# Optimization experiments

Hardware: AMD Instinct MI355X
Metric: run time of the kernel (lower is better)

Reference implementation:

```python
import jax, jax.numpy as jnp
import numpy as np

N_NODES = 50000
N_EDGES = 800000
IN, HID, OUT = 96, 96, 64


def setup_inputs() -> dict:
    key = jax.random.key(0)
    ks = jax.random.split(key, 12)
    x = jax.random.normal(ks[0], (N_NODES, IN), dtype=jnp.float32)
    src = jax.random.randint(ks[1], (N_EDGES,), 0, N_NODES, dtype=jnp.int32)
    dst = jax.random.randint(ks[2], (N_EDGES,), 0, N_NODES, dtype=jnp.int32)
    dims = [(IN, HID), (HID, HID), (HID, OUT)]
    params = {}
    for i, (din, dout) in enumerate(dims):
        s = 1.0 / np.sqrt(din)
        params[f"w_self{i}"] = jax.random.uniform(ks[3 + 3 * i], (dout, din), jnp.float32, -s, s)
        params[f"w_neigh{i}"] = jax.random.uniform(ks[4 + 3 * i], (dout, din), jnp.float32, -s, s)
        params[f"b{i}"] = jnp.zeros((dout,), jnp.float32)
    return {"x": x, "src": src, "dst": dst, **params}


def _sage_layer(h, src, dst, w_self, w_neigh, b):
    # mean aggregation of source-node features onto destination nodes
    msum = jax.ops.segment_sum(h[src], dst, num_segments=N_NODES)  # [N, d]
    deg = jax.ops.segment_sum(jnp.ones((src.shape[0],), h.dtype), dst, num_segments=N_NODES)
    hmean = msum / jnp.maximum(deg, 1.0)[:, None]
    return h @ w_self.T + hmean @ w_neigh.T + b


def reference(x, src, dst,
              w_self0, w_neigh0, b0,
              w_self1, w_neigh1, b1,
              w_self2, w_neigh2, b2):
    # Layer 0 + ReLU (dropout is identity in eval mode)
    h = jax.nn.relu(_sage_layer(x, src, dst, w_self0, w_neigh0, b0))
    # Layer 1 + ReLU
    h = jax.nn.relu(_sage_layer(h, src, dst, w_self1, w_neigh1, b1))
    # Final layer, no activation
    h = _sage_layer(h, src, dst, w_self2, w_neigh2, b2)
    return h
```

## Files before the change

### kernel.cpp

```cpp
#include <hip/hip_runtime.h>
#include <hip/hip_fp16.h>


#define DIN 96

typedef __attribute__((ext_vector_type(8))) short bf16x8;
typedef __attribute__((ext_vector_type(16))) float f32x16;

__global__ void zero_deg_kernel(int* __restrict__ p, int n) {
    int i = blockIdx.x * blockDim.x + threadIdx.x;
    if (i < n) p[i] = 0;
}

__global__ void deg_kernel(const int* __restrict__ dst, int* __restrict__ deg,
                           int* __restrict__ rank, int nE) {
    int i = blockIdx.x * blockDim.x + threadIdx.x;
    if (i < nE) rank[i] = atomicAdd(&deg[dst[i]], 1);
}

__global__ void block_sum_kernel(const int* __restrict__ deg, int* __restrict__ bsum, int nN) {
    __shared__ int s[256];
    const int tid = threadIdx.x;
    int i = blockIdx.x * 256 + tid;
    s[tid] = (i < nN) ? deg[i] : 0;
    __syncthreads();
    for (int d = 128; d > 0; d >>= 1) {
        if (tid < d) s[tid] += s[tid + d];
        __syncthreads();
    }
    if (tid == 0) bsum[blockIdx.x] = s[0];
}

__global__ void bsum_scan_kernel(int* __restrict__ bsum, int nB) {
    __shared__ int s[256];
    const int tid = threadIdx.x;
    int v = (tid < nB) ? bsum[tid] : 0;
    s[tid] = v;
    __syncthreads();
    for (int d = 1; d < 256; d <<= 1) {
        int t = (tid >= d) ? s[tid - d] : 0;
        __syncthreads();
        s[tid] += t;
        __syncthreads();
    }
    if (tid < nB) bsum[tid] = s[tid] - v;
}

__global__ void scan_apply_kernel(const int* __restrict__ deg, const int* __restrict__ bsum,
                                  int* __restrict__ offs, int nN) {
    __shared__ int s[256];
    const int tid = threadIdx.x;
    int i = blockIdx.x * 256 + tid;
    int v = (i < nN) ? deg[i] : 0;
    s[tid] = v;
    __syncthreads();
    for (int d = 1; d < 256; d <<= 1) {
        int t = (tid >= d) ? s[tid - d] : 0;
        __syncthreads();
        s[tid] += t;
        __syncthreads();
    }
    if (i < nN) offs[i] = bsum[blockIdx.x] + s[tid] - v;
}

__global__ void bucket_kernel(const int* __restrict__ src, const int* __restrict__ dst,
                              const int* __restrict__ offs, const int* __restrict__ rank,
                              unsigned short* __restrict__ esrc, int nE) {
    int e = blockIdx.x * blockDim.x + threadIdx.x;
    if (e < nE) esrc[offs[dst[e]] + rank[e]] = (unsigned short)src[e];
}

__global__ void tof16_kernel(const float* __restrict__ x, __half* __restrict__ xf, int n8) {
    int i = blockIdx.x * blockDim.x + threadIdx.x;
    if (i >= n8) return;
    float4 f0 = *reinterpret_cast<const float4*>(x + (size_t)i * 8);
    float4 f1 = *reinterpret_cast<const float4*>(x + (size_t)i * 8 + 4);
    union { __half2 h2[4]; float4 raw; } o;
    o.h2[0] = __float22half2_rn(make_float2(f0.x, f0.y));
    o.h2[1] = __float22half2_rn(make_float2(f0.z, f0.w));
    o.h2[2] = __float22half2_rn(make_float2(f1.x, f1.y));
    o.h2[3] = __float22half2_rn(make_float2(f1.z, f1.w));
    *reinterpret_cast<float4*>(xf + (size_t)i * 8) = o.raw;
}

__global__ void gather_kernel(const __half* __restrict__ hf, const unsigned short* __restrict__ esrc,
                              const int* __restrict__ offs, const int* __restrict__ deg,
                              float* __restrict__ hmean, int nN) {
    int idx = blockIdx.x * blockDim.x + threadIdx.x;
    if (idx >= nN * 12) return;
    int n = idx / 12;
    int q = idx - n * 12;
    const int beg = offs[n];
    const int dg = deg[n];
    const int end = beg + dg;
    const __half* hq = hf + q * 8;

    union H8 { float4 raw; __half2 h2[4]; };
    float a0[8], a1[8], a2[8], a3[8];
#pragma unroll
    for (int k = 0; k < 8; ++k) { a0[k] = 0.f; a1[k] = 0.f; a2[k] = 0.f; a3[k] = 0.f; }

    int j = beg;
    for (; j + 4 <= end; j += 4) {
        int s0 = esrc[j], s1 = esrc[j + 1], s2 = esrc[j + 2], s3 = esrc[j + 3];
        H8 v0, v1, v2, v3;
        v0.raw = *reinterpret_cast<const float4*>(hq + (size_t)s0 * DIN);
        v1.raw = *reinterpret_cast<const float4*>(hq + (size_t)s1 * DIN);
        v2.raw = *reinterpret_cast<const float4*>(hq + (size_t)s2 * DIN);
        v3.raw = *reinterpret_cast<const float4*>(hq + (size_t)s3 * DIN);
#pragma unroll
        for (int k = 0; k < 4; ++k) {
            float2 f0 = __half22float2(v0.h2[k]);
            float2 f1 = __half22float2(v1.h2[k]);
            float2 f2 = __half22float2(v2.h2[k]);
            float2 f3 = __half22float2(v3.h2[k]);
            a0[2 * k] += f0.x; a0[2 * k + 1] += f0.y;
            a1[2 * k] += f1.x; a1[2 * k + 1] += f1.y;
            a2[2 * k] += f2.x; a2[2 * k + 1] += f2.y;
            a3[2 * k] += f3.x; a3[2 * k + 1] += f3.y;
        }
    }
    for (; j < end; ++j) {
        int s0 = esrc[j];
        H8 v0;
        v0.raw = *reinterpret_cast<const float4*>(hq + (size_t)s0 * DIN);
#pragma unroll
        for (int k = 0; k < 4; ++k) {
            float2 f0 = __half22float2(v0.h2[k]);
            a0[2 * k] += f0.x; a0[2 * k + 1] += f0.y;
        }
    }
    const float r = 1.0f / (float)max(dg, 1);
    float4 o0, o1;
    o0.x = (a0[0] + a1[0] + a2[0] + a3[0]) * r;
    o0.y = (a0[1] + a1[1] + a2[1] + a3[1]) * r;
    o0.z = (a0[2] + a1[2] + a2[2] + a3[2]) * r;
    o0.w = (a0[3] + a1[3] + a2[3] + a3[3]) * r;
    o1.x = (a0[4] + a1[4] + a2[4] + a3[4]) * r;
    o1.y = (a0[5] + a1[5] + a2[5] + a3[5]) * r;
    o1.z = (a0[6] + a1[6] + a2[6] + a3[6]) * r;
    o1.w = (a0[7] + a1[7] + a2[7] + a3[7]) * r;
    float* op = hmean + (size_t)n * DIN + q * 8;
    *reinterpret_cast<float4*>(op) = o0;
    *reinterpret_cast<float4*>(op + 4) = o1;
}

__device__ __forceinline__ void f32x8_to_hilo(const float4 f0, const float4 f1,
                                              bf16x8& hi, bf16x8& lo) {
    union { unsigned int u[4]; bf16x8 v; } H, L;
    const float fv[8] = {f0.x, f0.y, f0.z, f0.w, f1.x, f1.y, f1.z, f1.w};
#pragma unroll
    for (int i = 0; i < 4; ++i) {
        unsigned u0 = __float_as_uint(fv[2 * i]);
        unsigned u1 = __float_as_uint(fv[2 * i + 1]);
        unsigned h0 = u0 & 0xFFFF0000u;
        unsigned h1 = u1 & 0xFFFF0000u;
        H.u[i] = h1 | (h0 >> 16);
        float l0 = fv[2 * i]     - __uint_as_float(h0);
        float l1 = fv[2 * i + 1] - __uint_as_float(h1);
        L.u[i] = (__float_as_uint(l1) & 0xFFFF0000u) | (__float_as_uint(l0) >> 16);
    }
    hi = H.v; lo = L.v;
}

template<int DOUT, bool RELU, bool WF16>
__global__ __launch_bounds__(256)
void sage_gemm_mfma(const float* __restrict__ hin, const float* __restrict__ hmean,
                    const float* __restrict__ wself, const float* __restrict__ wneigh,
                    const float* __restrict__ bias, float* __restrict__ hout,
                    __half* __restrict__ fout, int nN) {
    __shared__ unsigned int WhiS[32][100];
    __shared__ unsigned int WloS[32][100];

    const int tid = threadIdx.x;
    const int n0 = blockIdx.x * 256;
    const int ob = blockIdx.y * 32;

    for (int c = tid; c < 32 * 24; c += 256) {
        int r = c / 24, k8 = c - (c / 24) * 24;
        const float* srcw = (k8 < 12) ? (wself + (size_t)(ob + r) * 96 + k8 * 8)
                                      : (wneigh + (size_t)(ob + r) * 96 + (k8 - 12) * 8);
        float4 f0 = *reinterpret_cast<const float4*>(srcw);
        float4 f1 = *reinterpret_cast<const float4*>(srcw + 4);
        bf16x8 hi, lo;
        f32x8_to_hilo(f0, f1, hi, lo);
        *reinterpret_cast<bf16x8*>(&WhiS[r][k8 * 4]) = hi;
        *reinterpret_cast<bf16x8*>(&WloS[r][k8 * 4]) = lo;
    }
    __syncthreads();

    const int lane = tid & 63;
    const int w = tid >> 6;
    const int col = lane & 31;
    const int q = lane >> 5;
    const int mbase = n0 + w * 64;

    const int nA0 = min(mbase + col, nN - 1);
    const int nA1 = min(mbase + 32 + col, nN - 1);

    f32x16 acc0 = {};
    f32x16 acc1 = {};

#pragma unroll
    for (int ks = 0; ks < 12; ++ks) {
        const int kk = ks * 16 + q * 8;
        const float* s0;
        const float* s1;
        if (kk < 96) {
            s0 = hin + (size_t)nA0 * 96 + kk;
            s1 = hin + (size_t)nA1 * 96 + kk;
        } else {
            s0 = hmean + (size_t)nA0 * 96 + (kk - 96);
            s1 = hmean + (size_t)nA1 * 96 + (kk - 96);
        }
        float4 a00 = *reinterpret_cast<const float4*>(s0);
        float4 a01 = *reinterpret_cast<const float4*>(s0 + 4);
        float4 a10 = *reinterpret_cast<const float4*>(s1);
        float4 a11 = *reinterpret_cast<const float4*>(s1 + 4);
        bf16x8 ahi0, alo0, ahi1, alo1;
        f32x8_to_hilo(a00, a01, ahi0, alo0);
        f32x8_to_hilo(a10, a11, ahi1, alo1);

        const bf16x8 whi = *reinterpret_cast<const bf16x8*>(&WhiS[col][ks * 8 + q * 4]);
        const bf16x8 wlo = *reinterpret_cast<const bf16x8*>(&WloS[col][ks * 8 + q * 4]);

        acc0 = __builtin_amdgcn_mfma_f32_32x32x16_bf16(ahi0, whi, acc0, 0, 0, 0);
        acc0 = __builtin_amdgcn_mfma_f32_32x32x16_bf16(ahi0, wlo, acc0, 0, 0, 0);
        acc0 = __builtin_amdgcn_mfma_f32_32x32x16_bf16(alo0, whi, acc0, 0, 0, 0);
        acc1 = __builtin_amdgcn_mfma_f32_32x32x16_bf16(ahi1, whi, acc1, 0, 0, 0);
        acc1 = __builtin_amdgcn_mfma_f32_32x32x16_bf16(ahi1, wlo, acc1, 0, 0, 0);
        acc1 = __builtin_amdgcn_mfma_f32_32x32x16_bf16(alo1, whi, acc1, 0, 0, 0);
    }

    const float bv = bias[ob + col];
#pragma unroll
    for (int i = 0; i < 16; ++i) {
        const int row = (i & 3) + 8 * (i >> 2) + 4 * q;
        int n = mbase + row;
        if (n < nN) {
            float v = acc0[i] + bv;
            if (RELU) v = fmaxf(v, 0.f);
            hout[(size_t)n * DOUT + ob + col] = v;
            if (WF16) fout[(size_t)n * DOUT + ob + col] = __float2half_rn(v);
        }
        n = mbase + 32 + row;
        if (n < nN) {
            float v = acc1[i] + bv;
            if (RELU) v = fmaxf(v, 0.f);
            hout[(size_t)n * DOUT + ob + col] = v;
            if (WF16) fout[(size_t)n * DOUT + ob + col] = __float2half_rn(v);
        }
    }
}

extern "C" void kernel_launch(void* const* d_in, const int* in_sizes, int n_in,
                              void* d_out, int out_size, void* d_ws, size_t ws_size,
                              hipStream_t stream) {
    const float* x   = (const float*)d_in[0];
    const int*   src = (const int*)d_in[1];
    const int*   dst = (const int*)d_in[2];
    const float* ws0 = (const float*)d_in[3];
    const float* wn0 = (const float*)d_in[4];
    const float* b0  = (const float*)d_in[5];
    const float* ws1 = (const float*)d_in[6];
    const float* wn1 = (const float*)d_in[7];
    const float* b1  = (const float*)d_in[8];
    const float* ws2 = (const float*)d_in[9];
    const float* wn2 = (const float*)d_in[10];
    const float* b2  = (const float*)d_in[11];
    float* out = (float*)d_out;

    const int nN = in_sizes[0] / DIN;
    const int nE = in_sizes[1];
    const int nB = (nN + 255) / 256;

    int* deg  = (int*)d_ws;
    int* offs = deg + 50048;
    int* bsum = offs + 50048;
    int* rank = bsum + 256;
    unsigned short* esrc = (unsigned short*)(rank + nE);
    float* hmean = (float*)(esrc + nE);
    float* hA    = hmean + (size_t)nN * DIN;
    float* hB    = hA + (size_t)nN * DIN;

    __half* f16buf = (__half*)d_out;

    zero_deg_kernel<<<nB, 256, 0, stream>>>(deg, nN);
    deg_kernel<<<(nE + 255) / 256, 256, 0, stream>>>(dst, deg, rank, nE);
    block_sum_kernel<<<nB, 256, 0, stream>>>(deg, bsum, nN);
    bsum_scan_kernel<<<1, 256, 0, stream>>>(bsum, nB);
    scan_apply_kernel<<<nB, 256, 0, stream>>>(deg, bsum, offs, nN);
    bucket_kernel<<<(nE + 255) / 256, 256, 0, stream>>>(src, dst, offs, rank, esrc, nE);

    const int ggrid = (nN * 12 + 255) / 256;
    const int cgrid = (nN * 12 + 255) / 256;
    const int mblocks = (nN + 255) / 256;
    dim3 mgrid96(mblocks, 3);
    dim3 mgrid64(mblocks, 2);

    tof16_kernel<<<cgrid, 256, 0, stream>>>(x, f16buf, nN * 12);
    gather_kernel<<<ggrid, 256, 0, stream>>>(f16buf, esrc, offs, deg, hmean, nN);
    sage_gemm_mfma<96, true, true><<<mgrid96, 256, 0, stream>>>(x, hmean, ws0, wn0, b0, hA, f16buf, nN);

    gather_kernel<<<ggrid, 256, 0, stream>>>(f16buf, esrc, offs, deg, hmean, nN);
    sage_gemm_mfma<96, true, true><<<mgrid96, 256, 0, stream>>>(hA, hmean, ws1, wn1, b1, hB, f16buf, nN);

    gather_kernel<<<ggrid, 256, 0, stream>>>(f16buf, esrc, offs, deg, hmean, nN);
    sage_gemm_mfma<64, false, false><<<mgrid64, 256, 0, stream>>>(hB, hmean, ws2, wn2, b2, out, nullptr, nN);
}
```

Measured before the change: 228.2 us.

## Store neighbour mean in fp16 and compute all output columns per GEMM block

The gather kernel now writes the mean-aggregated features as fp16 instead of fp32, which halves its store traffic and the GEMM's hmean reads. The GEMM no longer splits output columns across blockIdx.y. Each block loads the full weight matrix into LDS and loops over all 32-column panels, so every A row is read and split into hi/lo parts once instead of 2-3 times. The cost is rounding the mean to fp16 before the bf16 hi/lo split, larger LDS use, more accumulator registers, and fewer blocks in flight.

```diff
diff --git a/kernel.cpp b/kernel.cpp
--- a/kernel.cpp
+++ b/kernel.cpp
@@ -85,7 +85,7 @@
 
 __global__ void gather_kernel(const __half* __restrict__ hf, const unsigned short* __restrict__ esrc,
                               const int* __restrict__ offs, const int* __restrict__ deg,
-                              float* __restrict__ hmean, int nN) {
+                              __half* __restrict__ hmean, int nN) {
     int idx = blockIdx.x * blockDim.x + threadIdx.x;
     if (idx >= nN * 12) return;
     int n = idx / 12;
@@ -131,24 +131,16 @@
         }
     }
     const float r = 1.0f / (float)max(dg, 1);
-    float4 o0, o1;
-    o0.x = (a0[0] + a1[0] + a2[0] + a3[0]) * r;
-    o0.y = (a0[1] + a1[1] + a2[1] + a3[1]) * r;
-    o0.z = (a0[2] + a1[2] + a2[2] + a3[2]) * r;
-    o0.w = (a0[3] + a1[3] + a2[3] + a3[3]) * r;
-    o1.x = (a0[4] + a1[4] + a2[4] + a3[4]) * r;
-    o1.y = (a0[5] + a1[5] + a2[5] + a3[5]) * r;
-    o1.z = (a0[6] + a1[6] + a2[6] + a3[6]) * r;
-    o1.w = (a0[7] + a1[7] + a2[7] + a3[7]) * r;
-    float* op = hmean + (size_t)n * DIN + q * 8;
-    *reinterpret_cast<float4*>(op) = o0;
-    *reinterpret_cast<float4*>(op + 4) = o1;
-}
-
-__device__ __forceinline__ void f32x8_to_hilo(const float4 f0, const float4 f1,
-                                              bf16x8& hi, bf16x8& lo) {
+    union H8 o;
+    o.h2[0] = __float22half2_rn(make_float2((a0[0]+a1[0]+a2[0]+a3[0])*r, (a0[1]+a1[1]+a2[1]+a3[1])*r));
+    o.h2[1] = __float22half2_rn(make_float2((a0[2]+a1[2]+a2[2]+a3[2])*r, (a0[3]+a1[3]+a2[3]+a3[3])*r));
+    o.h2[2] = __float22half2_rn(make_float2((a0[4]+a1[4]+a2[4]+a3[4])*r, (a0[5]+a1[5]+a2[5]+a3[5])*r));
+    o.h2[3] = __float22half2_rn(make_float2((a0[6]+a1[6]+a2[6]+a3[6])*r, (a0[7]+a1[7]+a2[7]+a3[7])*r));
+    *reinterpret_cast<float4*>(hmean + (size_t)n * DIN + q * 8) = o.raw;
+}
+
+__device__ __forceinline__ void fv8_to_hilo(const float* fv, bf16x8& hi, bf16x8& lo) {
     union { unsigned int u[4]; bf16x8 v; } H, L;
-    const float fv[8] = {f0.x, f0.y, f0.z, f0.w, f1.x, f1.y, f1.z, f1.w};
 #pragma unroll
     for (int i = 0; i < 4; ++i) {
         unsigned u0 = __float_as_uint(fv[2 * i]);
@@ -163,27 +155,27 @@
     hi = H.v; lo = L.v;
 }
 
-template<int DOUT, bool RELU, bool WF16>
+template<int DOUT, int NP, bool RELU, bool WF16>
 __global__ __launch_bounds__(256)
-void sage_gemm_mfma(const float* __restrict__ hin, const float* __restrict__ hmean,
+void sage_gemm_mfma(const float* __restrict__ hin, const __half* __restrict__ hm16,
                     const float* __restrict__ wself, const float* __restrict__ wneigh,
                     const float* __restrict__ bias, float* __restrict__ hout,
                     __half* __restrict__ fout, int nN) {
-    __shared__ unsigned int WhiS[32][100];
-    __shared__ unsigned int WloS[32][100];
+    __shared__ unsigned int WhiS[DOUT][100];
+    __shared__ unsigned int WloS[DOUT][100];
 
     const int tid = threadIdx.x;
     const int n0 = blockIdx.x * 256;
-    const int ob = blockIdx.y * 32;
-
-    for (int c = tid; c < 32 * 24; c += 256) {
+
+    for (int c = tid; c < DOUT * 24; c += 256) {
         int r = c / 24, k8 = c - (c / 24) * 24;
-        const float* srcw = (k8 < 12) ? (wself + (size_t)(ob + r) * 96 + k8 * 8)
-                                      : (wneigh + (size_t)(ob + r) * 96 + (k8 - 12) * 8);
+        const float* srcw = (k8 < 12) ? (wself + (size_t)r * 96 + k8 * 8)
+                                      : (wneigh + (size_t)r * 96 + (k8 - 12) * 8);
         float4 f0 = *reinterpret_cast<const float4*>(srcw);
         float4 f1 = *reinterpret_cast<const float4*>(srcw + 4);
+        float fv[8] = {f0.x, f0.y, f0.z, f0.w, f1.x, f1.y, f1.z, f1.w};
         bf16x8 hi, lo;
-        f32x8_to_hilo(f0, f1, hi, lo);
+        fv8_to_hilo(fv, hi, lo);
         *reinterpret_cast<bf16x8*>(&WhiS[r][k8 * 4]) = hi;
         *reinterpret_cast<bf16x8*>(&WloS[r][k8 * 4]) = lo;
     }
@@ -198,57 +190,80 @@
     const int nA0 = min(mbase + col, nN - 1);
     const int nA1 = min(mbase + 32 + col, nN - 1);
 
-    f32x16 acc0 = {};
-    f32x16 acc1 = {};
+    f32x16 acc[NP][2];
+#pragma unroll
+    for (int p = 0; p < NP; ++p) {
+        f32x16 z = {};
+        acc[p][0] = z;
+        acc[p][1] = z;
+    }
 
 #pragma unroll
     for (int ks = 0; ks < 12; ++ks) {
-        const int kk = ks * 16 + q * 8;
-        const float* s0;
-        const float* s1;
-        if (kk < 96) {
-            s0 = hin + (size_t)nA0 * 96 + kk;
-            s1 = hin + (size_t)nA1 * 96 + kk;
+        float fv0[8], fv1[8];
+        if (ks < 6) {
+            const float* s0 = hin + (size_t)nA0 * 96 + ks * 16 + q * 8;
+            const float* s1 = hin + (size_t)nA1 * 96 + ks * 16 + q * 8;
+            float4 a = *reinterpret_cast<const float4*>(s0);
+            float4 b = *reinterpret_cast<const float4*>(s0 + 4);
+            float4 c = *reinterpret_cast<const float4*>(s1);
+            float4 d = *reinterpret_cast<const float4*>(s1 + 4);
+            fv0[0]=a.x; fv0[1]=a.y; fv0[2]=a.z; fv0[3]=a.w;
+            fv0[4]=b.x; fv0[5]=b.y; fv0[6]=b.z; fv0[7]=b.w;
+            fv1[0]=c.x; fv1[1]=c.y; fv1[2]=c.z; fv1[3]=c.w;
+            fv1[4]=d.x; fv1[5]=d.y; fv1[6]=d.z; fv1[7]=d.w;
         } else {
-            s0 = hmean + (size_t)nA0 * 96 + (kk - 96);
-            s1 = hmean + (size_t)nA1 * 96 + (kk - 96);
-        }
-        float4 a00 = *reinterpret_cast<const float4*>(s0);
-        float4 a01 = *reinterpret_cast<const float4*>(s0 + 4);
-        float4 a10 = *reinterpret_cast<const float4*>(s1);
-        float4 a11 = *reinterpret_cast<const float4*>(s1 + 4);
+            const __half* s0 = hm16 + (size_t)nA0 * 96 + (ks - 6) * 16 + q * 8;
+            const __half* s1 = hm16 + (size_t)nA1 * 96 + (ks - 6) * 16 + q * 8;
+            union { float4 raw; __half2 h2[4]; } u0, u1;
+            u0.raw = *reinterpret_cast<const float4*>(s0);
+            u1.raw = *reinterpret_cast<const float4*>(s1);
+#pragma unroll
+            for (int k = 0; k < 4; ++k) {
+                float2 f0 = __half22float2(u0.h2[k]);
+                float2 f1 = __half22float2(u1.h2[k]);
+                fv0[2 * k] = f0.x; fv0[2 * k + 1] = f0.y;
+                fv1[2 * k] = f1.x; fv1[2 * k + 1] = f1.y;
+            }
+        }
         bf16x8 ahi0, alo0, ahi1, alo1;
-        f32x8_to_hilo(a00, a01, ahi0, alo0);
-        f32x8_to_hilo(a10, a11, ahi1, alo1);
-
-        const bf16x8 whi = *reinterpret_cast<const bf16x8*>(&WhiS[col][ks * 8 + q * 4]);
-        const bf16x8 wlo = *reinterpret_cast<const bf16x8*>(&WloS[col][ks * 8 + q * 4]);
-
-        acc0 = __builtin_amdgcn_mfma_f32_32x32x16_bf16(ahi0, whi, acc0, 0, 0, 0);
-        acc0 = __builtin_amdgcn_mfma_f32_32x32x16_bf16(ahi0, wlo, acc0, 0, 0, 0);
-        acc0 = __builtin_amdgcn_mfma_f32_32x32x16_bf16(alo0, whi, acc0, 0, 0, 0);
-        acc1 = __builtin_amdgcn_mfma_f32_32x32x16_bf16(ahi1, whi, acc1, 0, 0, 0);
-        acc1 = __builtin_amdgcn_mfma_f32_32x32x16_bf16(ahi1, wlo, acc1, 0, 0, 0);
-        acc1 = __builtin_amdgcn_mfma_f32_32x32x16_bf16(alo1, whi, acc1, 0, 0, 0);
-    }
-
-    const float bv = bias[ob + col];
-#pragma unroll
-    for (int i = 0; i < 16; ++i) {
-        const int row = (i & 3) + 8 * (i >> 2) + 4 * q;
-        int n = mbase + row;
-        if (n < nN) {
-            float v = acc0[i] + bv;
-            if (RELU) v = fmaxf(v, 0.f);
-            hout[(size_t)n * DOUT + ob + col] = v;
-            if (WF16) fout[(size_t)n * DOUT + ob + col] = __float2half_rn(v);
-        }
-        n = mbase + 32 + row;
-        if (n < nN) {
-            float v = acc1[i] + bv;
-            if (RELU) v = fmaxf(v, 0.f);
-            hout[(size_t)n * DOUT + ob + col] = v;
-            if (WF16) fout[(size_t)n * DOUT + ob + col] = __float2half_rn(v);
+        fv8_to_hilo(fv0, ahi0, alo0);
+        fv8_to_hilo(fv1, ahi1, alo1);
+
+#pragma unroll
+        for (int p = 0; p < NP; ++p) {
+            const bf16x8 whi = *reinterpret_cast<const bf16x8*>(&WhiS[p * 32 + col][ks * 8 + q * 4]);
+            const bf16x8 wlo = *reinterpret_cast<const bf16x8*>(&WloS[p * 32 + col][ks * 8 + q * 4]);
+            acc[p][0] = __builtin_amdgcn_mfma_f32_32x32x16_bf16(ahi0, whi, acc[p][0], 0, 0, 0);
+            acc[p][0] = __builtin_amdgcn_mfma_f32_32x32x16_bf16(ahi0, wlo, acc[p][0], 0, 0, 0);
+            acc[p][0] = __builtin_amdgcn_mfma_f32_32x32x16_bf16(alo0, whi, acc[p][0], 0, 0, 0);
+            acc[p][1] = __builtin_amdgcn_mfma_f32_32x32x16_bf16(ahi1, whi, acc[p][1], 0, 0, 0);
+            acc[p][1] = __builtin_amdgcn_mfma_f32_32x32x16_bf16(ahi1, wlo, acc[p][1], 0, 0, 0);
+            acc[p][1] = __builtin_amdgcn_mfma_f32_32x32x16_bf16(alo1, whi, acc[p][1], 0, 0, 0);
+        }
+    }
+
+#pragma unroll
+    for (int p = 0; p < NP; ++p) {
+        const int oc = p * 32 + col;
+        const float bv = bias[oc];
+#pragma unroll
+        for (int i = 0; i < 16; ++i) {
+            const int row = (i & 3) + 8 * (i >> 2) + 4 * q;
+            int n = mbase + row;
+            if (n < nN) {
+                float v = acc[p][0][i] + bv;
+                if (RELU) v = fmaxf(v, 0.f);
+                hout[(size_t)n * DOUT + oc] = v;
+                if (WF16) fout[(size_t)n * DOUT + oc] = __float2half_rn(v);
+            }
+            n = mbase + 32 + row;
+            if (n < nN) {
+                float v = acc[p][1][i] + bv;
+                if (RELU) v = fmaxf(v, 0.f);
+                hout[(size_t)n * DOUT + oc] = v;
+                if (WF16) fout[(size_t)n * DOUT + oc] = __float2half_rn(v);
+            }
         }
     }
 }
@@ -279,8 +294,8 @@
     int* bsum = offs + 50048;
     int* rank = bsum + 256;
     unsigned short* esrc = (unsigned short*)(rank + nE);
-    float* hmean = (float*)(esrc + nE);
-    float* hA    = hmean + (size_t)nN * DIN;
+    __half* hm16 = (__half*)(esrc + nE);
+    float* hA    = (float*)(hm16 + (size_t)nN * DIN);
     float* hB    = hA + (size_t)nN * DIN;
 
     __half* f16buf = (__half*)d_out;
@@ -293,18 +308,15 @@
     bucket_kernel<<<(nE + 255) / 256, 256, 0, stream>>>(src, dst, offs, rank, esrc, nE);
 
     const int ggrid = (nN * 12 + 255) / 256;
-    const int cgrid = (nN * 12 + 255) / 256;
-    const int mblocks = (nN + 255) / 256;
-    dim3 mgrid96(mblocks, 3);
-    dim3 mgrid64(mblocks, 2);
-
-    tof16_kernel<<<cgrid, 256, 0, stream>>>(x, f16buf, nN * 12);
-    gather_kernel<<<ggrid, 256, 0, stream>>>(f16buf, esrc, offs, deg, hmean, nN);
-    sage_gemm_mfma<96, true, true><<<mgrid96, 256, 0, stream>>>(x, hmean, ws0, wn0, b0, hA, f16buf, nN);
-
-    gather_kernel<<<ggrid, 256, 0, stream>>>(f16buf, esrc, offs, deg, hmean, nN);
-    sage_gemm_mfma<96, true, true><<<mgrid96, 256, 0, stream>>>(hA, hmean, ws1, wn1, b1, hB, f16buf, nN);
-
-    gather_kernel<<<ggrid, 256, 0, stream>>>(f16buf, esrc, offs, deg, hmean, nN);
-    sage_gemm_mfma<64, false, false><<<mgrid64, 256, 0, stream>>>(hB, hmean, ws2, wn2, b2, out, nullptr, nN);
-}
+    const int mgrid = (nN + 255) / 256;
+
+    tof16_kernel<<<ggrid, 256, 0, stream>>>(x, f16buf, nN * 12);
+    gather_kernel<<<ggrid, 256, 0, stream>>>(f16buf, esrc, offs, deg, hm16, nN);
+    sage_gemm_mfma<96, 3, true, true><<<mgrid, 256, 0, stream>>>(x, hm16, ws0, wn0, b0, hA, f16buf, nN);
+
+    gather_kernel<<<ggrid, 256, 0, stream>>>(f16buf, esrc, offs, deg, hm16, nN);
+    sage_gemm_mfma<96, 3, true, true><<<mgrid, 256, 0, stream>>>(hA, hm16, ws1, wn1, b1, hB, f16buf, nN);
+
+    gather_kernel<<<ggrid, 256, 0, stream>>>(f16buf, esrc, offs, deg, hm16, nN);
+    sage_gemm_mfma<64, 2, false, false><<<mgrid, 256, 0, stream>>>(hB, hm16, ws2, wn2, b2, out, nullptr, nN);
+}
```

Result: faster. 222.8 us (-2.4%).
